# Kernel optimization log

Measured on AMD Instinct MI355X. Metric: run time of the kernel, lower is better.

The kernel has to match this reference:

```python
import jax, jax.numpy as jnp
import numpy as np

D = 1024      # total input features
R = 32        # number of ragged regions
RMAX = 32     # max region size (padding target)
HIDDEN = [128, 128]
H1, H2 = HIDDEN
B = 8192      # batch size


def _made_masks(r, rmax, hidden):
    """TFP AutoregressiveNetwork masks (left-to-right order, 'equal' hidden degrees,
    params=2, use_bias=False), zero-padded to rmax features."""
    order = np.arange(1, r + 1)
    degs = [order]
    for u in hidden:
        mn = min(int(degs[-1].min()), r - 1)
        degs.append(np.maximum(mn, np.ceil(np.arange(1, u + 1) * (r - 1) / float(u + 1)).astype(np.int64)))
    m1 = np.zeros((rmax, hidden[0]), bool)
    m1[:r] = degs[0][:, None] <= degs[1][None, :]
    m2 = degs[1][:, None] <= degs[2][None, :]
    mout = np.zeros((hidden[-1], rmax * 2), bool)
    out_deg = np.repeat(order, 2)  # output layout is feature-major: [feat, param]
    mout[:, :2 * r] = degs[-1][:, None] < out_deg[None, :]
    return m1, m2, mout


def setup_inputs() -> dict:
    rng = np.random.default_rng(0)
    perm = rng.permutation(D)
    sizes = rng.integers(8, RMAX + 1, size=R)
    idx = np.zeros((R, RMAX), np.int64)
    valid = np.zeros((R, RMAX), bool)
    M1 = np.zeros((R, RMAX, H1), bool)
    M2 = np.zeros((R, H1, H2), bool)
    Mout = np.zeros((R, H2, RMAX * 2), bool)
    pos = 0
    for i in range(R):
        s = int(sizes[i])
        idx[i, :s] = perm[pos:pos + s]
        pos += s
        valid[i, :s] = True
        M1[i], M2[i], Mout[i] = _made_masks(s, RMAX, HIDDEN)
    key = jax.random.key(0)
    k1, k2, k3, k4 = jax.random.split(key, 4)
    inputs = jax.random.normal(k1, (B, D), jnp.float32)
    W1 = jax.random.normal(k2, (R, RMAX, H1), jnp.float32) / np.float32(np.sqrt(RMAX))
    W2 = jax.random.normal(k3, (R, H1, H2), jnp.float32) / np.float32(np.sqrt(H1))
    Wout = jax.random.normal(k4, (R, H2, RMAX * 2), jnp.float32) / np.float32(np.sqrt(H2))
    return {"inputs": inputs, "W1": W1, "W2": W2, "Wout": Wout,
            "idx": jnp.asarray(idx), "valid": jnp.asarray(valid),
            "M1": jnp.asarray(M1), "M2": jnp.asarray(M2), "Mout": jnp.asarray(Mout)}


def reference(inputs, W1, W2, Wout, idx, valid, M1, M2, Mout):
    f = inputs.dtype
    v = valid.astype(f)                              # [R, RMAX]
    xg = jnp.take(inputs, idx, axis=1) * v           # [B, R, RMAX] ragged gather (padded)
    # MADE masked MLP (relu, no bias), batched over all regions at once
    h1 = jax.nn.relu(jnp.einsum('brd,rdh->brh', xg, W1 * M1.astype(f)))
    h2 = jax.nn.relu(jnp.einsum('brh,rhk->brk', h1, W2 * M2.astype(f)))
    out = jnp.einsum('brk,rko->bro', h2, Wout * Mout.astype(f))
    out = out.reshape(out.shape[0], out.shape[1], RMAX, 2)
    shift, log_s = out[..., 0], out[..., 1]
    # MAF inverse: u = (x - shift) * exp(-log_scale); logdet = -sum(log_scale)
    u = (xg - shift) * jnp.exp(-log_s)
    elem = -0.5 * u * u - 0.5 * jnp.log(2.0 * jnp.pi) - log_s
    ll = jnp.sum(elem * v, axis=-1)                  # [B, R]
    return ll[..., None]                             # [B, R, 1] as in tf.stack of expand_dims
```

## Files before the change

### kernel.cpp

```cpp
#include <hip/hip_runtime.h>
#include <math.h>


#define RR 32
#define DD 1024
#define HH 128
#define OO 64
#define TROWS 32
#define TILES_PER_BLOCK 8
#define BLOCKS_PER_R 32

#define SHP 136
#define SXG 40
#define SXF 38
#define SSC 136

typedef _Float16 f16x8_t __attribute__((ext_vector_type(8)));
typedef float f32x4_t __attribute__((ext_vector_type(4)));
typedef unsigned short u16;
typedef unsigned int u32;

__device__ __forceinline__ u16 f16b(float x) {
    _Float16 h = (_Float16)x;
    union { _Float16 f; u16 u; } c; c.f = h; return c.u;
}
__device__ __forceinline__ f32x4_t mfma16h(f16x8_t a, f16x8_t b, f32x4_t c) {
    return __builtin_amdgcn_mfma_f32_16x16x32_f16(a, b, c, 0, 0, 0);
}

__device__ __forceinline__ void stage_block16(const float* __restrict__ W,
                                              const int* __restrict__ M,
                                              int ldc, int c0, int K, u16* dst,
                                              int tid)
{
    const int kb = tid >> 3;
    const int cb = tid & 7;
    if (kb * 4 >= K) return;
    const int k0 = kb * 4;
    float e[4][4];
#pragma unroll
    for (int i = 0; i < 4; ++i) {
        const int o = ((k0 + i) * ldc + c0 + 4 * cb) >> 2;
        float4 w = ((const float4*)W)[o];
        int4   m = ((const int4*)M)[o];
        e[i][0] = m.x ? w.x : 0.f; e[i][1] = m.y ? w.y : 0.f;
        e[i][2] = m.z ? w.z : 0.f; e[i][3] = m.w ? w.w : 0.f;
    }
#pragma unroll
    for (int j = 0; j < 4; ++j) {
        ushort4 p;
        p.x = f16b(e[0][j]); p.y = f16b(e[1][j]);
        p.z = f16b(e[2][j]); p.w = f16b(e[3][j]);
        *(ushort4*)&dst[(4 * cb + j) * SSC + k0] = p;
    }
}

__device__ __forceinline__ void relu_store16(u16* __restrict__ dst, int o, f32x4_t a)
{
    ushort4 s;
    s.x = f16b(fmaxf(a[0], 0.f));
    s.y = f16b(fmaxf(a[1], 0.f));
    s.z = f16b(fmaxf(a[2], 0.f));
    s.w = f16b(fmaxf(a[3], 0.f));
    *(ushort4*)&dst[o] = s;
}

__global__ __launch_bounds__(512, 6)
void made_flow_r12(const float* __restrict__ inputs,
                   const float* __restrict__ W1,
                   const float* __restrict__ W2,
                   const float* __restrict__ Wout,
                   const int* __restrict__ idx,
                   const int* __restrict__ valid,
                   const int* __restrict__ M1,
                   const int* __restrict__ M2,
                   const int* __restrict__ Mout,
                   float* __restrict__ out)
{
    __shared__ __align__(16) char regA[TROWS * SHP * 2];
    __shared__ __align__(16) char regB[TROWS * SHP * 2];
    __shared__ __align__(16) u16  xgh[2][TROWS * SXG];
    __shared__ __align__(16) float xgf[2][TROWS * SXF];
    __shared__ __align__(16) float red_all[TILES_PER_BLOCK][TROWS][4];
    __shared__ int   idx_s[RR];
    __shared__ float v_s[RR];

    u16* const h1h  = (u16*)regA;
    u16* const scr  = (u16*)regA;
    u16* const scr2 = (u16*)regB;
    u16* const h2h  = (u16*)regB;

    const int tid  = threadIdx.x;
    const int r    = blockIdx.x / BLOCKS_PER_R;
    const int rb   = blockIdx.x % BLOCKS_PER_R;
    const int lane = tid & 63;
    const int wave = tid >> 6;
    const int q    = lane >> 4;
    const int l16  = lane & 15;
    const int wm3  = wave & 3;
    const int ni3  = wave >> 2;

    if (tid < RR) {
        idx_s[tid] = idx[r * RR + tid];
        v_s[tid]   = valid[r * RR + tid] ? 1.f : 0.f;
    }

    f16x8_t a1;
    f16x8_t a2[4];
    f16x8_t ao[4];
    {
        const float* W1r = W1 + r * RR * HH;   const int* M1r = M1 + r * RR * HH;
        const float* W2r = W2 + r * HH * HH;   const int* M2r = M2 + r * HH * HH;
        const float* Wor = Wout + r * HH * OO; const int* Mor = Mout + r * HH * OO;
        const int c = wave >> 1, h = wave & 1;
        for (int i = 0; i < 2; ++i) {
            __syncthreads();
            if (tid < 256) stage_block16(W2r, M2r, HH, 32 * (2 * i),     HH, scr,  tid);
            else           stage_block16(W2r, M2r, HH, 32 * (2 * i + 1), HH, scr2, tid - 256);
            __syncthreads();
            if (c == 2 * i) {
#pragma unroll
                for (int ks = 0; ks < 4; ++ks)
                    a2[ks] = *(const f16x8_t*)&scr[(16 * h + l16) * SSC + ks * 32 + q * 8];
            } else if (c == 2 * i + 1) {
#pragma unroll
                for (int ks = 0; ks < 4; ++ks)
                    a2[ks] = *(const f16x8_t*)&scr2[(16 * h + l16) * SSC + ks * 32 + q * 8];
            }
        }
        {
            __syncthreads();
            if (tid < 256) stage_block16(Wor, Mor, OO, 0,  HH, scr,  tid);
            else           stage_block16(Wor, Mor, OO, 32, HH, scr2, tid - 256);
            __syncthreads();
            const u16* s = (wm3 >> 1) ? scr2 : scr;
#pragma unroll
            for (int ks = 0; ks < 4; ++ks)
                ao[ks] = *(const f16x8_t*)&s[(16 * (wm3 & 1) + l16) * SSC + ks * 32 + q * 8];
        }
        for (int i = 0; i < 2; ++i) {
            __syncthreads();
            if (tid < 256) stage_block16(W1r, M1r, HH, 32 * (2 * i),     RR, scr,  tid);
            else           stage_block16(W1r, M1r, HH, 32 * (2 * i + 1), RR, scr2, tid - 256);
            __syncthreads();
            if (c == 2 * i)          a1 = *(const f16x8_t*)&scr [(16 * h + l16) * SSC + q * 8];
            else if (c == 2 * i + 1) a1 = *(const f16x8_t*)&scr2[(16 * h + l16) * SSC + q * 8];
        }
    }
    __syncthreads();

    const f32x4_t zero4 = {0.f, 0.f, 0.f, 0.f};
    const int grow = tid >> 4;
    const int gg   = tid & 15;

    const int   ci0 = idx_s[2 * gg], ci1 = idx_s[2 * gg + 1];
    const float cv0 = v_s[2 * gg],   cv1 = v_s[2 * gg + 1];
    const int   gbase = (rb * TILES_PER_BLOCK * TROWS + grow) * DD;

    {
        float gx0 = inputs[gbase + ci0] * cv0;
        float gx1 = inputs[gbase + ci1] * cv1;
        u32 p = (u32)f16b(gx0) | ((u32)f16b(gx1) << 16);
        *(u32*)&xgh[0][grow * SXG + 2 * gg] = p;
        *(float2*)&xgf[0][grow * SXF + 2 * gg] = make_float2(gx0, gx1);
    }
    __syncthreads();

    {
#pragma unroll
        for (int ni = 0; ni < 2; ++ni) {
            f16x8_t b = *(const f16x8_t*)&xgh[0][(16 * ni + l16) * SXG + q * 8];
            f32x4_t a = mfma16h(a1, b, zero4);
            relu_store16(h1h, (16 * ni + l16) * SHP + 16 * wave + 4 * q, a);
        }
    }

    float gx0, gx1;
    {
        gx0 = inputs[gbase + TROWS * DD + ci0] * cv0;
        gx1 = inputs[gbase + TROWS * DD + ci1] * cv1;
    }

    for (int t = 0; t < TILES_PER_BLOCK; ++t) {
        __syncthreads();

        const bool dg = (t + 1 < TILES_PER_BLOCK);
        {
            f32x4_t acc[2] = {zero4, zero4};
#pragma unroll
            for (int ks = 0; ks < 4; ++ks) {
#pragma unroll
                for (int ni = 0; ni < 2; ++ni) {
                    f16x8_t b = *(const f16x8_t*)&h1h[(16 * ni + l16) * SHP + ks * 32 + q * 8];
                    acc[ni] = mfma16h(a2[ks], b, acc[ni]);
                }
            }
            if (dg) {
                const int bb = (t + 1) & 1;
                u32 p = (u32)f16b(gx0) | ((u32)f16b(gx1) << 16);
                *(u32*)&xgh[bb][grow * SXG + 2 * gg] = p;
                *(float2*)&xgf[bb][grow * SXF + 2 * gg] = make_float2(gx0, gx1);
            }
#pragma unroll
            for (int ni = 0; ni < 2; ++ni)
                relu_store16(h2h, (16 * ni + l16) * SHP + 16 * wave + 4 * q, acc[ni]);
        }
        __syncthreads();

        if (t + 2 < TILES_PER_BLOCK) {
            const int base = gbase + (t + 2) * (TROWS * DD);
            gx0 = inputs[base + ci0] * cv0;
            gx1 = inputs[base + ci1] * cv1;
        }

        f32x4_t acc3 = zero4;
#pragma unroll
        for (int ks = 0; ks < 4; ++ks) {
            f16x8_t b = *(const f16x8_t*)&h2h[(16 * ni3 + l16) * SHP + ks * 32 + q * 8];
            acc3 = mfma16h(ao[ks], b, acc3);
        }

        if (dg) {
            const int bb = (t + 1) & 1;
#pragma unroll
            for (int ni = 0; ni < 2; ++ni) {
                f16x8_t b = *(const f16x8_t*)&xgh[bb][(16 * ni + l16) * SXG + q * 8];
                f32x4_t a = mfma16h(a1, b, zero4);
                relu_store16(h1h, (16 * ni + l16) * SHP + 16 * wave + 4 * q, a);
            }
        }

        {
            const int j0 = 8 * wm3 + 2 * q;
            const float vj0 = v_s[j0], vj1 = v_s[j0 + 1];
            const int row = 16 * ni3 + l16;
            float2 xv = *(const float2*)&xgf[t & 1][row * SXF + j0];
            const float u0 = (xv.x - acc3[0]) * __expf(-acc3[1]);
            const float u1 = (xv.y - acc3[2]) * __expf(-acc3[3]);
            float p = (-0.5f * u0 * u0 - 0.91893853320467266954f - acc3[1]) * vj0
                    + (-0.5f * u1 * u1 - 0.91893853320467266954f - acc3[3]) * vj1;
            p += __shfl_xor(p, 16, 64);
            p += __shfl_xor(p, 32, 64);
            if (q == 0) red_all[t][row][wm3] = p;
        }
    }

    __syncthreads();
    if (tid < TILES_PER_BLOCK * TROWS) {
        const int tt  = tid >> 5;
        const int row = tid & 31;
        float4 rv = *(const float4*)&red_all[tt][row][0];
        out[((rb * TILES_PER_BLOCK + tt) * TROWS + row) * RR + r] =
            rv.x + rv.y + rv.z + rv.w;
    }
}

extern "C" void kernel_launch(void* const* d_in, const int* in_sizes, int n_in,
                              void* d_out, int out_size, void* d_ws, size_t ws_size,
                              hipStream_t stream)
{
    const float* inputs = (const float*)d_in[0];
    const float* W1     = (const float*)d_in[1];
    const float* W2     = (const float*)d_in[2];
    const float* Wout   = (const float*)d_in[3];
    const int*   idx    = (const int*)d_in[4];
    const int*   valid  = (const int*)d_in[5];
    const int*   M1     = (const int*)d_in[6];
    const int*   M2     = (const int*)d_in[7];
    const int*   Mout   = (const int*)d_in[8];
    float*       out    = (float*)d_out;

    hipLaunchKernelGGL(made_flow_r12, dim3(RR * BLOCKS_PER_R), dim3(512), 0, stream,
                       inputs, W1, W2, Wout, idx, valid, M1, M2, Mout, out);
}
```

Before: 125.2 us.

## Software-pipeline MLP layers across tiles with double-buffered hidden states, one barrier per tile

```diff
diff --git a/kernel.cpp b/kernel.cpp
--- a/kernel.cpp
+++ b/kernel.cpp
@@ -12,7 +12,6 @@
 
 #define SHP 136
 #define SXG 40
-#define SXF 38
 #define SSC 136
 
 typedef _Float16 f16x8_t __attribute__((ext_vector_type(8)));
@@ -66,7 +65,7 @@
 }
 
 __global__ __launch_bounds__(512, 6)
-void made_flow_r12(const float* __restrict__ inputs,
+void made_flow_r13(const float* __restrict__ inputs,
                    const float* __restrict__ W1,
                    const float* __restrict__ W2,
                    const float* __restrict__ Wout,
@@ -77,18 +76,15 @@
                    const int* __restrict__ Mout,
                    float* __restrict__ out)
 {
-    __shared__ __align__(16) char regA[TROWS * SHP * 2];
-    __shared__ __align__(16) char regB[TROWS * SHP * 2];
-    __shared__ __align__(16) u16  xgh[2][TROWS * SXG];
-    __shared__ __align__(16) float xgf[2][TROWS * SXF];
+    __shared__ __align__(16) u16 h1s[2][TROWS * SHP];
+    __shared__ __align__(16) u16 h2s[2][TROWS * SHP];
+    __shared__ __align__(16) u16 xgh[4][TROWS * SXG];
     __shared__ __align__(16) float red_all[TILES_PER_BLOCK][TROWS][4];
     __shared__ int   idx_s[RR];
     __shared__ float v_s[RR];
 
-    u16* const h1h  = (u16*)regA;
-    u16* const scr  = (u16*)regA;
-    u16* const scr2 = (u16*)regB;
-    u16* const h2h  = (u16*)regB;
+    u16* const scr  = h1s[0];
+    u16* const scr2 = h1s[1];
 
     const int tid  = threadIdx.x;
     const int r    = blockIdx.x / BLOCKS_PER_R;
@@ -158,11 +154,12 @@
     const int   gbase = (rb * TILES_PER_BLOCK * TROWS + grow) * DD;
 
     {
-        float gx0 = inputs[gbase + ci0] * cv0;
-        float gx1 = inputs[gbase + ci1] * cv1;
-        u32 p = (u32)f16b(gx0) | ((u32)f16b(gx1) << 16);
-        *(u32*)&xgh[0][grow * SXG + 2 * gg] = p;
-        *(float2*)&xgf[0][grow * SXF + 2 * gg] = make_float2(gx0, gx1);
+        float a0 = inputs[gbase + ci0] * cv0;
+        float a1v = inputs[gbase + ci1] * cv1;
+        float b0 = inputs[gbase + TROWS * DD + ci0] * cv0;
+        float b1 = inputs[gbase + TROWS * DD + ci1] * cv1;
+        *(u32*)&xgh[0][grow * SXG + 2 * gg] = (u32)f16b(a0) | ((u32)f16b(a1v) << 16);
+        *(u32*)&xgh[1][grow * SXG + 2 * gg] = (u32)f16b(b0) | ((u32)f16b(b1) << 16);
     }
     __syncthreads();
 
@@ -171,77 +168,82 @@
         for (int ni = 0; ni < 2; ++ni) {
             f16x8_t b = *(const f16x8_t*)&xgh[0][(16 * ni + l16) * SXG + q * 8];
             f32x4_t a = mfma16h(a1, b, zero4);
-            relu_store16(h1h, (16 * ni + l16) * SHP + 16 * wave + 4 * q, a);
-        }
-    }
-
-    float gx0, gx1;
-    {
-        gx0 = inputs[gbase + TROWS * DD + ci0] * cv0;
-        gx1 = inputs[gbase + TROWS * DD + ci1] * cv1;
-    }
-
-    for (int t = 0; t < TILES_PER_BLOCK; ++t) {
+            relu_store16(h1s[0], (16 * ni + l16) * SHP + 16 * wave + 4 * q, a);
+        }
+    }
+
+    for (int t = 0; t <= TILES_PER_BLOCK; ++t) {
         __syncthreads();
 
-        const bool dg = (t + 1 < TILES_PER_BLOCK);
-        {
-            f32x4_t acc[2] = {zero4, zero4};
-#pragma unroll
-            for (int ks = 0; ks < 4; ++ks) {
-#pragma unroll
-                for (int ni = 0; ni < 2; ++ni) {
-                    f16x8_t b = *(const f16x8_t*)&h1h[(16 * ni + l16) * SHP + ks * 32 + q * 8];
-                    acc[ni] = mfma16h(a2[ks], b, acc[ni]);
-                }
-            }
-            if (dg) {
-                const int bb = (t + 1) & 1;
-                u32 p = (u32)f16b(gx0) | ((u32)f16b(gx1) << 16);
-                *(u32*)&xgh[bb][grow * SXG + 2 * gg] = p;
-                *(float2*)&xgf[bb][grow * SXF + 2 * gg] = make_float2(gx0, gx1);
-            }
-#pragma unroll
-            for (int ni = 0; ni < 2; ++ni)
-                relu_store16(h2h, (16 * ni + l16) * SHP + 16 * wave + 4 * q, acc[ni]);
-        }
-        __syncthreads();
-
-        if (t + 2 < TILES_PER_BLOCK) {
+        const bool doP2  = (t < TILES_PER_BLOCK);
+        const bool doP3  = (t >= 1);
+        const bool doP1n = (t + 1 < TILES_PER_BLOCK);
+        const bool doG   = (t + 2 < TILES_PER_BLOCK);
+
+        float gx0, gx1;
+        if (doG) {
             const int base = gbase + (t + 2) * (TROWS * DD);
             gx0 = inputs[base + ci0] * cv0;
             gx1 = inputs[base + ci1] * cv1;
         }
 
         f32x4_t acc3 = zero4;
-#pragma unroll
-        for (int ks = 0; ks < 4; ++ks) {
-            f16x8_t b = *(const f16x8_t*)&h2h[(16 * ni3 + l16) * SHP + ks * 32 + q * 8];
-            acc3 = mfma16h(ao[ks], b, acc3);
-        }
-
-        if (dg) {
-            const int bb = (t + 1) & 1;
+        if (doP3) {
+            const u16* h2b = h2s[(t - 1) & 1];
+#pragma unroll
+            for (int ks = 0; ks < 4; ++ks) {
+                f16x8_t b = *(const f16x8_t*)&h2b[(16 * ni3 + l16) * SHP + ks * 32 + q * 8];
+                acc3 = mfma16h(ao[ks], b, acc3);
+            }
+        }
+
+        if (doP2) {
+            const u16* h1b = h1s[t & 1];
+            u16*       h2b = h2s[t & 1];
+            f32x4_t acc[2] = {zero4, zero4};
+#pragma unroll
+            for (int ks = 0; ks < 4; ++ks) {
+#pragma unroll
+                for (int ni = 0; ni < 2; ++ni) {
+                    f16x8_t b = *(const f16x8_t*)&h1b[(16 * ni + l16) * SHP + ks * 32 + q * 8];
+                    acc[ni] = mfma16h(a2[ks], b, acc[ni]);
+                }
+            }
+#pragma unroll
+            for (int ni = 0; ni < 2; ++ni)
+                relu_store16(h2b, (16 * ni + l16) * SHP + 16 * wave + 4 * q, acc[ni]);
+        }
+
+        if (doP1n) {
+            const u16* xb  = xgh[(t + 1) & 3];
+            u16*       h1b = h1s[(t + 1) & 1];
 #pragma unroll
             for (int ni = 0; ni < 2; ++ni) {
-                f16x8_t b = *(const f16x8_t*)&xgh[bb][(16 * ni + l16) * SXG + q * 8];
+                f16x8_t b = *(const f16x8_t*)&xb[(16 * ni + l16) * SXG + q * 8];
                 f32x4_t a = mfma16h(a1, b, zero4);
-                relu_store16(h1h, (16 * ni + l16) * SHP + 16 * wave + 4 * q, a);
-            }
-        }
-
-        {
+                relu_store16(h1b, (16 * ni + l16) * SHP + 16 * wave + 4 * q, a);
+            }
+        }
+
+        if (doP3) {
             const int j0 = 8 * wm3 + 2 * q;
             const float vj0 = v_s[j0], vj1 = v_s[j0 + 1];
             const int row = 16 * ni3 + l16;
-            float2 xv = *(const float2*)&xgf[t & 1][row * SXF + j0];
-            const float u0 = (xv.x - acc3[0]) * __expf(-acc3[1]);
-            const float u1 = (xv.y - acc3[2]) * __expf(-acc3[3]);
+            u32 xw = *(const u32*)&xgh[(t - 1) & 3][row * SXG + j0];
+            union { u32 u; _Float16 h[2]; } xc; xc.u = xw;
+            const float xv0 = (float)xc.h[0], xv1 = (float)xc.h[1];
+            const float u0 = (xv0 - acc3[0]) * __expf(-acc3[1]);
+            const float u1 = (xv1 - acc3[2]) * __expf(-acc3[3]);
             float p = (-0.5f * u0 * u0 - 0.91893853320467266954f - acc3[1]) * vj0
                     + (-0.5f * u1 * u1 - 0.91893853320467266954f - acc3[3]) * vj1;
             p += __shfl_xor(p, 16, 64);
             p += __shfl_xor(p, 32, 64);
-            if (q == 0) red_all[t][row][wm3] = p;
+            if (q == 0) red_all[t - 1][row][wm3] = p;
+        }
+
+        if (doG) {
+            *(u32*)&xgh[(t + 2) & 3][grow * SXG + 2 * gg] =
+                (u32)f16b(gx0) | ((u32)f16b(gx1) << 16);
         }
     }
 
@@ -270,6 +272,6 @@
     const int*   Mout   = (const int*)d_in[8];
     float*       out    = (float*)d_out;
 
-    hipLaunchKernelGGL(made_flow_r12, dim3(RR * BLOCKS_PER_R), dim3(512), 0, stream,
+    hipLaunchKernelGGL(made_flow_r13, dim3(RR * BLOCKS_PER_R), dim3(512), 0, stream,
                        inputs, W1, W2, Wout, idx, valid, M1, M2, Mout, out);
 }
```

New measurement: 125.1 us. About the same (-0.1%).

## Shrink LDS footprint and raise occupancy target to eight blocks

Applied to the files above, without the earlier changes.

```diff
diff --git a/kernel.cpp b/kernel.cpp
--- a/kernel.cpp
+++ b/kernel.cpp
@@ -12,7 +12,6 @@
 
 #define SHP 136
 #define SXG 40
-#define SXF 38
 #define SSC 136
 
 typedef _Float16 f16x8_t __attribute__((ext_vector_type(8)));
@@ -65,8 +64,8 @@
     *(ushort4*)&dst[o] = s;
 }
 
-__global__ __launch_bounds__(512, 6)
-void made_flow_r12(const float* __restrict__ inputs,
+__global__ __launch_bounds__(512, 8)
+void made_flow_r15(const float* __restrict__ inputs,
                    const float* __restrict__ W1,
                    const float* __restrict__ W2,
                    const float* __restrict__ Wout,
@@ -77,18 +76,13 @@
                    const int* __restrict__ Mout,
                    float* __restrict__ out)
 {
-    __shared__ __align__(16) char regA[TROWS * SHP * 2];
-    __shared__ __align__(16) char regB[TROWS * SHP * 2];
-    __shared__ __align__(16) u16  xgh[2][TROWS * SXG];
-    __shared__ __align__(16) float xgf[2][TROWS * SXF];
-    __shared__ __align__(16) float red_all[TILES_PER_BLOCK][TROWS][4];
-    __shared__ int   idx_s[RR];
-    __shared__ float v_s[RR];
-
-    u16* const h1h  = (u16*)regA;
-    u16* const scr  = (u16*)regA;
-    u16* const scr2 = (u16*)regB;
-    u16* const h2h  = (u16*)regB;
+    __shared__ __align__(16) u16 h1s[TROWS * SHP];
+    __shared__ __align__(16) u16 h2s[TROWS * SHP];
+    __shared__ __align__(16) u16 xgh[2][TROWS * SXG];
+    __shared__ __align__(16) float red2[2][TROWS][4];
+
+    u16* const scr  = h1s;
+    u16* const scr2 = h2s;
 
     const int tid  = threadIdx.x;
     const int r    = blockIdx.x / BLOCKS_PER_R;
@@ -100,10 +94,15 @@
     const int wm3  = wave & 3;
     const int ni3  = wave >> 2;
 
-    if (tid < RR) {
-        idx_s[tid] = idx[r * RR + tid];
-        v_s[tid]   = valid[r * RR + tid] ? 1.f : 0.f;
-    }
+    const int grow = tid >> 4;
+    const int gg   = tid & 15;
+    const int   ci0 = idx[r * RR + 2 * gg];
+    const int   ci1 = idx[r * RR + 2 * gg + 1];
+    const float cv0 = valid[r * RR + 2 * gg]     ? 1.f : 0.f;
+    const float cv1 = valid[r * RR + 2 * gg + 1] ? 1.f : 0.f;
+    const int j0  = 8 * wm3 + 2 * q;
+    const float vj0 = valid[r * RR + j0]     ? 1.f : 0.f;
+    const float vj1 = valid[r * RR + j0 + 1] ? 1.f : 0.f;
 
     f16x8_t a1;
     f16x8_t a2[4];
@@ -150,19 +149,15 @@
     __syncthreads();
 
     const f32x4_t zero4 = {0.f, 0.f, 0.f, 0.f};
-    const int grow = tid >> 4;
-    const int gg   = tid & 15;
-
-    const int   ci0 = idx_s[2 * gg], ci1 = idx_s[2 * gg + 1];
-    const float cv0 = v_s[2 * gg],   cv1 = v_s[2 * gg + 1];
-    const int   gbase = (rb * TILES_PER_BLOCK * TROWS + grow) * DD;
-
+    const int gbase = (rb * TILES_PER_BLOCK * TROWS + grow) * DD;
+
+    float gx0, gx1;
     {
-        float gx0 = inputs[gbase + ci0] * cv0;
-        float gx1 = inputs[gbase + ci1] * cv1;
-        u32 p = (u32)f16b(gx0) | ((u32)f16b(gx1) << 16);
-        *(u32*)&xgh[0][grow * SXG + 2 * gg] = p;
-        *(float2*)&xgf[0][grow * SXF + 2 * gg] = make_float2(gx0, gx1);
+        float a0 = inputs[gbase + ci0] * cv0;
+        float a1v = inputs[gbase + ci1] * cv1;
+        *(u32*)&xgh[0][grow * SXG + 2 * gg] = (u32)f16b(a0) | ((u32)f16b(a1v) << 16);
+        gx0 = inputs[gbase + TROWS * DD + ci0] * cv0;
+        gx1 = inputs[gbase + TROWS * DD + ci1] * cv1;
     }
     __syncthreads();
 
@@ -171,39 +166,37 @@
         for (int ni = 0; ni < 2; ++ni) {
             f16x8_t b = *(const f16x8_t*)&xgh[0][(16 * ni + l16) * SXG + q * 8];
             f32x4_t a = mfma16h(a1, b, zero4);
-            relu_store16(h1h, (16 * ni + l16) * SHP + 16 * wave + 4 * q, a);
-        }
-    }
-
-    float gx0, gx1;
-    {
-        gx0 = inputs[gbase + TROWS * DD + ci0] * cv0;
-        gx1 = inputs[gbase + TROWS * DD + ci1] * cv1;
+            relu_store16(h1s, (16 * ni + l16) * SHP + 16 * wave + 4 * q, a);
+        }
     }
 
     for (int t = 0; t < TILES_PER_BLOCK; ++t) {
         __syncthreads();
 
         const bool dg = (t + 1 < TILES_PER_BLOCK);
+
+        if (dg) {
+            *(u32*)&xgh[(t + 1) & 1][grow * SXG + 2 * gg] =
+                (u32)f16b(gx0) | ((u32)f16b(gx1) << 16);
+        }
         {
             f32x4_t acc[2] = {zero4, zero4};
 #pragma unroll
             for (int ks = 0; ks < 4; ++ks) {
 #pragma unroll
                 for (int ni = 0; ni < 2; ++ni) {
-                    f16x8_t b = *(const f16x8_t*)&h1h[(16 * ni + l16) * SHP + ks * 32 + q * 8];
+                    f16x8_t b = *(const f16x8_t*)&h1s[(16 * ni + l16) * SHP + ks * 32 + q * 8];
                     acc[ni] = mfma16h(a2[ks], b, acc[ni]);
                 }
             }
-            if (dg) {
-                const int bb = (t + 1) & 1;
-                u32 p = (u32)f16b(gx0) | ((u32)f16b(gx1) << 16);
-                *(u32*)&xgh[bb][grow * SXG + 2 * gg] = p;
-                *(float2*)&xgf[bb][grow * SXF + 2 * gg] = make_float2(gx0, gx1);
-            }
 #pragma unroll
             for (int ni = 0; ni < 2; ++ni)
-                relu_store16(h2h, (16 * ni + l16) * SHP + 16 * wave + 4 * q, acc[ni]);
+                relu_store16(h2s, (16 * ni + l16) * SHP + 16 * wave + 4 * q, acc[ni]);
+        }
+        if (t >= 2 && tid < TROWS) {
+            float4 rv = *(const float4*)&red2[t & 1][tid][0];
+            out[((rb * TILES_PER_BLOCK + (t - 2)) * TROWS + tid) * RR + r] =
+                rv.x + rv.y + rv.z + rv.w;
         }
         __syncthreads();
 
@@ -216,40 +209,39 @@
         f32x4_t acc3 = zero4;
 #pragma unroll
         for (int ks = 0; ks < 4; ++ks) {
-            f16x8_t b = *(const f16x8_t*)&h2h[(16 * ni3 + l16) * SHP + ks * 32 + q * 8];
+            f16x8_t b = *(const f16x8_t*)&h2s[(16 * ni3 + l16) * SHP + ks * 32 + q * 8];
             acc3 = mfma16h(ao[ks], b, acc3);
         }
 
         if (dg) {
-            const int bb = (t + 1) & 1;
 #pragma unroll
             for (int ni = 0; ni < 2; ++ni) {
-                f16x8_t b = *(const f16x8_t*)&xgh[bb][(16 * ni + l16) * SXG + q * 8];
+                f16x8_t b = *(const f16x8_t*)&xgh[(t + 1) & 1][(16 * ni + l16) * SXG + q * 8];
                 f32x4_t a = mfma16h(a1, b, zero4);
-                relu_store16(h1h, (16 * ni + l16) * SHP + 16 * wave + 4 * q, a);
+                relu_store16(h1s, (16 * ni + l16) * SHP + 16 * wave + 4 * q, a);
             }
         }
 
         {
-            const int j0 = 8 * wm3 + 2 * q;
-            const float vj0 = v_s[j0], vj1 = v_s[j0 + 1];
             const int row = 16 * ni3 + l16;
-            float2 xv = *(const float2*)&xgf[t & 1][row * SXF + j0];
-            const float u0 = (xv.x - acc3[0]) * __expf(-acc3[1]);
-            const float u1 = (xv.y - acc3[2]) * __expf(-acc3[3]);
+            u32 xw = *(const u32*)&xgh[t & 1][row * SXG + j0];
+            union { u32 u; _Float16 h[2]; } xc; xc.u = xw;
+            const float xv0 = (float)xc.h[0], xv1 = (float)xc.h[1];
+            const float u0 = (xv0 - acc3[0]) * __expf(-acc3[1]);
+            const float u1 = (xv1 - acc3[2]) * __expf(-acc3[3]);
             float p = (-0.5f * u0 * u0 - 0.91893853320467266954f - acc3[1]) * vj0
                     + (-0.5f * u1 * u1 - 0.91893853320467266954f - acc3[3]) * vj1;
             p += __shfl_xor(p, 16, 64);
             p += __shfl_xor(p, 32, 64);
-            if (q == 0) red_all[t][row][wm3] = p;
+            if (q == 0) red2[t & 1][row][wm3] = p;
         }
     }
 
     __syncthreads();
-    if (tid < TILES_PER_BLOCK * TROWS) {
-        const int tt  = tid >> 5;
+    if (tid < 2 * TROWS) {
+        const int tt  = TILES_PER_BLOCK - 2 + (tid >> 5);
         const int row = tid & 31;
-        float4 rv = *(const float4*)&red_all[tt][row][0];
+        float4 rv = *(const float4*)&red2[tt & 1][row][0];
         out[((rb * TILES_PER_BLOCK + tt) * TROWS + row) * RR + r] =
             rv.x + rv.y + rv.z + rv.w;
     }
@@ -270,6 +262,6 @@
     const int*   Mout   = (const int*)d_in[8];
     float*       out    = (float*)d_out;
 
-    hipLaunchKernelGGL(made_flow_r12, dim3(RR * BLOCKS_PER_R), dim3(512), 0, stream,
+    hipLaunchKernelGGL(made_flow_r15, dim3(RR * BLOCKS_PER_R), dim3(512), 0, stream,
                        inputs, W1, W2, Wout, idx, valid, M1, M2, Mout, out);
 }
```

After: 164.5 us. 1.31x slower.
